# Kernel tuning notes

Hardware: AMD Instinct MI355X
Metric: run time of the kernel (lower is better)

The kernel has to match this reference:

```python
import jax, jax.numpy as jnp
import numpy as np

N_NODES = 100000
N_EDGES = 1600000
IN_DIM, HID_DIM, LAT_DIM = 256, 128, 64


def setup_inputs() -> dict:
    key = jax.random.key(0)
    ks = jax.random.split(key, 10)
    x = jax.random.normal(ks[0], (N_NODES, IN_DIM), dtype=jnp.float32)
    edge_index = jax.random.randint(ks[1], (2, N_EDGES), 0, N_NODES, dtype=jnp.int32)
    s = 1.0 / np.sqrt(IN_DIM)
    W1 = jax.random.normal(ks[2], (IN_DIM, HID_DIM), dtype=jnp.float32) * s
    b1 = jnp.zeros((HID_DIM,), dtype=jnp.float32)
    s2 = 1.0 / np.sqrt(HID_DIM)
    Wmu = jax.random.normal(ks[3], (HID_DIM, LAT_DIM), dtype=jnp.float32) * s2
    bmu = jnp.zeros((LAT_DIM,), dtype=jnp.float32)
    Wls = jax.random.normal(ks[4], (HID_DIM, LAT_DIM), dtype=jnp.float32) * s2
    bls = jnp.zeros((LAT_DIM,), dtype=jnp.float32)
    eps = jax.random.normal(ks[5], (N_NODES, LAT_DIM), dtype=jnp.float32)
    return {"x": x, "edge_index": edge_index, "W1": W1, "b1": b1,
            "Wmu": Wmu, "bmu": bmu, "Wls": Wls, "bls": bls, "eps": eps}


def _gcn_norm(edge_index, n_nodes):
    # PyG GCNConv: add self-loops, symmetric normalization D^-1/2 A D^-1/2
    loops = jnp.arange(n_nodes, dtype=edge_index.dtype)
    src = jnp.concatenate([edge_index[0], loops])
    dst = jnp.concatenate([edge_index[1], loops])
    ones = jnp.ones(src.shape[0], dtype=jnp.float32)
    deg = jax.ops.segment_sum(ones, dst, num_segments=n_nodes)
    dinv = jnp.where(deg > 0, jax.lax.rsqrt(deg), 0.0)
    norm = dinv[src] * dinv[dst]  # [E + N]
    return src, dst, norm


def _gcn_conv(x, src, dst, norm, W, b, n_nodes):
    h = x @ W                       # transform first (in_dim >= out_dim)
    msg = h[src] * norm[:, None]    # gather + scale per edge
    out = jax.ops.segment_sum(msg, dst, num_segments=n_nodes)  # scatter-add
    return out + b


def reference(x, edge_index, W1, b1, Wmu, bmu, Wls, bls, eps):
    n = x.shape[0]
    src, dst, norm = _gcn_norm(edge_index, n)
    hidden = jax.nn.relu(_gcn_conv(x, src, dst, norm, W1, b1, n))
    mu = _gcn_conv(hidden, src, dst, norm, Wmu, bmu, n)
    logstd = _gcn_conv(hidden, src, dst, norm, Wls, bls, n)
    # reparameterize (training mode): z = mu + eps * exp(logstd)
    z = mu + eps * jnp.exp(logstd)
    return (z, mu, logstd)
```

## Files before the change

kernel.cpp:

```cpp
#include <hip/hip_runtime.h>
#include <cstdint>
#include <cstddef>

typedef __attribute__((ext_vector_type(8))) short short8v;
typedef __attribute__((ext_vector_type(4))) float f32x4;

#define BSHIFT 9
#define NBUCK_MAX 256
#define BCAP 16384
#define F8SCALE 16.0f
#define F8INV   0.0625f

__device__ __forceinline__ unsigned short f2bf_rne(float x) {
    unsigned int u = __float_as_uint(x);
    return (unsigned short)((u + 0x7fffu + ((u >> 16) & 1u)) >> 16);
}

__device__ __forceinline__ short8v pack_bf16x8(float4 a, float4 b) {
    unsigned int u0, u1, u2, u3;
    asm("v_cvt_pk_bf16_f32 %0, %1, %2" : "=v"(u0) : "v"(a.x), "v"(a.y));
    asm("v_cvt_pk_bf16_f32 %0, %1, %2" : "=v"(u1) : "v"(a.z), "v"(a.w));
    asm("v_cvt_pk_bf16_f32 %0, %1, %2" : "=v"(u2) : "v"(b.x), "v"(b.y));
    asm("v_cvt_pk_bf16_f32 %0, %1, %2" : "=v"(u3) : "v"(b.z), "v"(b.w));
    uint4 r = make_uint4(u0, u1, u2, u3);
    return *(short8v*)&r;
}

__device__ __forceinline__ unsigned int pk_fp8(float a, float b, float c, float d) {
    int r = 0;
    r = __builtin_amdgcn_cvt_pk_fp8_f32(a, b, r, false);
    r = __builtin_amdgcn_cvt_pk_fp8_f32(c, d, r, true);
    return (unsigned int)r;
}
__device__ __forceinline__ void accf8(float* a, uint2 v) {
    auto p0 = __builtin_amdgcn_cvt_pk_f32_fp8((int)v.x, false);
    auto p1 = __builtin_amdgcn_cvt_pk_f32_fp8((int)v.x, true);
    auto p2 = __builtin_amdgcn_cvt_pk_f32_fp8((int)v.y, false);
    auto p3 = __builtin_amdgcn_cvt_pk_f32_fp8((int)v.y, true);
    a[0] += p0[0]; a[1] += p0[1];
    a[2] += p1[0]; a[3] += p1[1];
    a[4] += p2[0]; a[5] += p2[1];
    a[6] += p3[0]; a[7] += p3[1];
}


__global__ __launch_bounds__(256) void k_prepB(const float* __restrict__ W1,
                                               const float* __restrict__ Wmu,
                                               const float* __restrict__ Wls,
                                               unsigned short* __restrict__ B1h,
                                               unsigned short* __restrict__ B2t,
                                               int* __restrict__ bcur) {
    int i = blockIdx.x * 256 + threadIdx.x;
    if (blockIdx.x == 0 && threadIdx.x < NBUCK_MAX) bcur[threadIdx.x] = 0;
    if (i < 256 * 128) {
        int k = i >> 7, c = i & 127;
        int ch = ((c & 15) << 3) | (c >> 4);
        B1h[c * 256 + k] = f2bf_rne(W1[k * 128 + ch]);
    }
    if (i < 128 * 128) {
        int k = i >> 7, och = i & 127;
        float vv = (och < 64) ? Wmu[k * 64 + och] : Wls[k * 64 + (och - 64)];
        B2t[och * 128 + k] = f2bf_rne(vv);
    }
}


__global__ __launch_bounds__(256) void k_scatb(const int* __restrict__ srcv,
                                               const int* __restrict__ dstv,
                                               int* __restrict__ bcur,
                                               unsigned int* __restrict__ ebuf, int E) {
    __shared__ int hcnt[NBUCK_MAX], hbase[NBUCK_MAX], hcur[NBUCK_MAX];
    int t = threadIdx.x;
    for (int b = t; b < NBUCK_MAX; b += 256) { hcnt[b] = 0; hcur[b] = 0; }
    __syncthreads();
    int base = blockIdx.x * 4096;
    for (int q = 0; q < 16; ++q) {
        int i = base + q * 256 + t;
        if (i < E) atomicAdd(&hcnt[dstv[i] >> BSHIFT], 1);
    }
    __syncthreads();
    for (int b = t; b < NBUCK_MAX; b += 256)
        hbase[b] = hcnt[b] ? atomicAdd(&bcur[b], hcnt[b]) : 0;
    __syncthreads();
    for (int q = 0; q < 16; ++q) {
        int i = base + q * 256 + t;
        if (i < E) {
            int d = dstv[i], b = d >> BSHIFT;
            int off = hbase[b] + atomicAdd(&hcur[b], 1);
            if (off < BCAP)
                ebuf[(size_t)b * BCAP + off] = ((unsigned)srcv[i] << 9) | (unsigned)(d & 511);
        }
    }
}

__global__ __launch_bounds__(512) void k_bsort(const unsigned int* __restrict__ ebuf,
                                               const int* __restrict__ bcur,
                                               int* __restrict__ colv,
                                               int* __restrict__ rowstart,
                                               int* __restrict__ rowend,
                                               float* __restrict__ dinv, int n) {
    __shared__ int cnt[512], sc[512], cur[512];
    int t = threadIdx.x;
    int b = blockIdx.x;
    int node0 = b << BSHIFT;
    int nn = min(512, n - node0);
    int s0 = (int)((size_t)b * BCAP);
    int total = min(bcur[b], BCAP);
    cnt[t] = 0;
    __syncthreads();
    for (int i = t; i < total; i += 512)
        atomicAdd(&cnt[ebuf[s0 + i] & 511u], 1);
    __syncthreads();
    int v = cnt[t];
    sc[t] = v;
    __syncthreads();
    for (int off = 1; off < 512; off <<= 1) {
        int x = 0;
        if (t >= off) x = sc[t - off];
        __syncthreads();
        if (t >= off) sc[t] += x;
        __syncthreads();
    }
    if (t < nn) {
        int rs = s0 + sc[t] - v;
        cur[t] = rs;
        rowstart[node0 + t] = rs;
        rowend[node0 + t] = rs + v;
        dinv[node0 + t] = rsqrtf((float)(v + 1));
    }
    __syncthreads();
    for (int i = t; i < total; i += 512) {
        unsigned int pv = ebuf[s0 + i];
        int pos = atomicAdd(&cur[pv & 511u], 1);
        colv[pos] = (int)(pv >> 9);
    }
}


__global__ __launch_bounds__(256) void k_gemm1(const float* __restrict__ A,
                                               const unsigned short* __restrict__ Bth,
                                               const float* __restrict__ dinv,
                                               unsigned char* __restrict__ Cf8, int M) {
    const int K = 256;
    __shared__ unsigned short Bs[128 * 128];
    const int tid = threadIdx.x;
    const int w = tid >> 6, l = tid & 63;
    const int lr = l & 15, lq = l >> 4;
    const int row0 = blockIdx.x * 64 + w * 16;

    int rg = row0 + lr;
    const float* ap = A + (size_t)(rg < M ? rg : 0) * K + lq * 8;

    float4 ar[8][2];
#pragma unroll
    for (int s = 0; s < 8; ++s) {
        ar[s][0] = *(const float4*)(ap + s * 32);
        ar[s][1] = *(const float4*)(ap + s * 32 + 4);
    }

    f32x4 acc[8];
#pragma unroll
    for (int ct = 0; ct < 8; ++ct) acc[ct] = (f32x4){0.f, 0.f, 0.f, 0.f};

#pragma unroll
    for (int h = 0; h < 2; ++h) {
        if (h) __syncthreads();
#pragma unroll
        for (int r = 0; r < 8; ++r) {
            int rw = r * 4 + w;
            int sl = rw >> 3, ct = rw & 7;
            short8v v = *(const short8v*)(Bth + (size_t)(ct * 16 + lr) * K + (h * 4 + sl) * 32 + lq * 8);
            *(short8v*)(&Bs[(rw * 64 + l) * 8]) = v;
        }
        __syncthreads();

#pragma unroll
        for (int sl = 0; sl < 4; ++sl) {
            int sg = h * 4 + sl;
            short8v ah = pack_bf16x8(ar[sg][0], ar[sg][1]);
#pragma unroll
            for (int ct = 0; ct < 8; ++ct) {
                short8v bh = *(const short8v*)(&Bs[((sl * 8 + ct) * 64 + l) * 8]);
                acc[ct] = __builtin_amdgcn_mfma_f32_16x16x32_bf16(ah, bh, acc[ct], 0, 0, 0);
            }
        }
    }

    int rbase = row0 + (lq << 2);
#pragma unroll
    for (int j = 0; j < 4; ++j) {
        int row = rbase + j;
        if (row < M) {
            float dv = dinv[row] * F8SCALE;
            uint2 r;
            r.x = pk_fp8(dv * acc[0][j], dv * acc[1][j], dv * acc[2][j], dv * acc[3][j]);
            r.y = pk_fp8(dv * acc[4][j], dv * acc[5][j], dv * acc[6][j], dv * acc[7][j]);
            *(uint2*)(Cf8 + (size_t)row * 128 + lr * 8) = r;
        }
    }
}


__global__ __launch_bounds__(256) void k_prop1(const unsigned char* __restrict__ hf,
                                               const int* __restrict__ colv,
                                               const int* __restrict__ rowstart,
                                               const int* __restrict__ rowend,
                                               const float* __restrict__ dinv,
                                               const float* __restrict__ bias,
                                               unsigned char* __restrict__ of, int n) {
    int wid = (blockIdx.x * 256 + threadIdx.x) >> 6;
    int nid = wid * 4 + ((threadIdx.x >> 4) & 3);
    if (nid >= n) return;
    int cl = threadIdx.x & 15;
    const unsigned char* hp = hf + cl * 8;
    int s = rowstart[nid], e = rowend[nid];
    float a[8] = {0.f, 0.f, 0.f, 0.f, 0.f, 0.f, 0.f, 0.f};
    int i = s;
    for (; i + 4 <= e; i += 4) {
        int c0 = colv[i], c1 = colv[i + 1], c2 = colv[i + 2], c3 = colv[i + 3];
        uint2 v0 = *(const uint2*)(hp + (size_t)c0 * 128);
        uint2 v1 = *(const uint2*)(hp + (size_t)c1 * 128);
        uint2 v2 = *(const uint2*)(hp + (size_t)c2 * 128);
        uint2 v3 = *(const uint2*)(hp + (size_t)c3 * 128);
        accf8(a, v0); accf8(a, v1); accf8(a, v2); accf8(a, v3);
    }
    for (; i < e; ++i) {
        int c = colv[i];
        uint2 v = *(const uint2*)(hp + (size_t)c * 128);
        accf8(a, v);
    }
    uint2 vo = *(const uint2*)(hp + (size_t)nid * 128);
    accf8(a, vo);
    float dv = dinv[nid];
    float din = dv * F8INV;
    float dos = dv * F8SCALE;
    float4 b0 = *(const float4*)(bias + cl * 8);
    float4 b1v = *(const float4*)(bias + cl * 8 + 4);
    float bb[8] = {b0.x, b0.y, b0.z, b0.w, b1v.x, b1v.y, b1v.z, b1v.w};
    float o[8];
#pragma unroll
    for (int k = 0; k < 8; ++k)
        o[k] = fmaxf(a[k] * din + bb[k], 0.f) * dos;
    uint2 r;
    r.x = pk_fp8(o[0], o[1], o[2], o[3]);
    r.y = pk_fp8(o[4], o[5], o[6], o[7]);
    *(uint2*)(of + (size_t)nid * 128 + cl * 8) = r;
}


__global__ __launch_bounds__(256) void k_prop2z(const unsigned char* __restrict__ hf,
                                                const int* __restrict__ colv,
                                                const int* __restrict__ rowstart,
                                                const int* __restrict__ rowend,
                                                const float* __restrict__ dinv,
                                                const unsigned short* __restrict__ B2t,
                                                const float* __restrict__ bmu,
                                                const float* __restrict__ bls,
                                                const float* __restrict__ eps,
                                                float* __restrict__ zout,
                                                float* __restrict__ muout,
                                                float* __restrict__ lsout, int n) {
    __shared__ unsigned short aggb[16][136];
    const int tid = threadIdx.x;
    const int w = tid >> 6, l = tid & 63;
    const int base = blockIdx.x * 16;

    {
        int g = l >> 4, cl = l & 15;
        int slot = w * 4 + g;
        int nid = base + slot;
        float a[8] = {0.f, 0.f, 0.f, 0.f, 0.f, 0.f, 0.f, 0.f};
        float dv = 0.f;
        if (nid < n) {
            const unsigned char* hp = hf + cl * 8;
            int s = rowstart[nid], e = rowend[nid];
            int i = s;
            for (; i + 4 <= e; i += 4) {
                int c0 = colv[i], c1 = colv[i + 1], c2 = colv[i + 2], c3 = colv[i + 3];
                uint2 v0 = *(const uint2*)(hp + (size_t)c0 * 128);
                uint2 v1 = *(const uint2*)(hp + (size_t)c1 * 128);
                uint2 v2 = *(const uint2*)(hp + (size_t)c2 * 128);
                uint2 v3 = *(const uint2*)(hp + (size_t)c3 * 128);
                accf8(a, v0); accf8(a, v1); accf8(a, v2); accf8(a, v3);
            }
            for (; i < e; ++i) {
                int c = colv[i];
                uint2 v = *(const uint2*)(hp + (size_t)c * 128);
                accf8(a, v);
            }
            uint2 vo = *(const uint2*)(hp + (size_t)nid * 128);
            accf8(a, vo);
            dv = dinv[nid] * F8INV;
        }
        short8v r;
#pragma unroll
        for (int k = 0; k < 8; ++k) r[k] = (short)f2bf_rne(a[k] * dv);
        *(short8v*)(&aggb[slot][cl * 8]) = r;
    }
    __syncthreads();

    const int lr = l & 15, lq = l >> 4;
    f32x4 acc0 = (f32x4){0.f, 0.f, 0.f, 0.f};
    f32x4 acc1 = (f32x4){0.f, 0.f, 0.f, 0.f};
#pragma unroll
    for (int sl = 0; sl < 4; ++sl) {
        short8v af = *(const short8v*)(&aggb[lr][sl * 32 + lq * 8]);
        short8v b0 = *(const short8v*)(B2t + (size_t)(w * 16 + lr) * 128 + sl * 32 + lq * 8);
        short8v b1 = *(const short8v*)(B2t + (size_t)((w + 4) * 16 + lr) * 128 + sl * 32 + lq * 8);
        acc0 = __builtin_amdgcn_mfma_f32_16x16x32_bf16(af, b0, acc0, 0, 0, 0);
        acc1 = __builtin_amdgcn_mfma_f32_16x16x32_bf16(af, b1, acc1, 0, 0, 0);
    }

    int och = w * 16 + lr;
    float bmv = bmu[och], blv = bls[och];
#pragma unroll
    for (int j = 0; j < 4; ++j) {
        int nid = base + lq * 4 + j;
        if (nid < n) {
            float mu = acc0[j] + bmv;
            float ls = acc1[j] + blv;
            size_t o = (size_t)nid * 64 + och;
            float z = mu + eps[o] * __expf(ls);
            zout[o] = z;
            muout[o] = mu;
            lsout[o] = ls;
        }
    }
}


extern "C" void kernel_launch(void* const* d_in, const int* in_sizes, int n_in,
                              void* d_out, int out_size, void* d_ws, size_t ws_size,
                              hipStream_t stream) {
    const float* x   = (const float*)d_in[0];
    const int*   ei  = (const int*)d_in[1];
    const float* W1  = (const float*)d_in[2];
    const float* b1  = (const float*)d_in[3];
    const float* Wmu = (const float*)d_in[4];
    const float* bmu = (const float*)d_in[5];
    const float* Wls = (const float*)d_in[6];
    const float* bls = (const float*)d_in[7];
    const float* eps = (const float*)d_in[8];

    const int n = in_sizes[0] / 256;
    const int E = in_sizes[1] / 2;
    const int* srcv = ei;
    const int* dstv = ei + E;
    const int nbuck = (n + 511) >> BSHIFT;

    char* w = (char*)d_ws;
    auto alloc = [&](size_t bytes) -> char* {
        char* p = w;
        w += (bytes + 255) & ~(size_t)255;
        return p;
    };
    float* dinv     = (float*)alloc((size_t)n * 4);
    int*   rowstart = (int*)alloc((size_t)n * 4);
    int*   rowend   = (int*)alloc((size_t)n * 4);
    int*   bcur     = (int*)alloc((size_t)NBUCK_MAX * 4);
    unsigned int* ebuf = (unsigned int*)alloc((size_t)nbuck * BCAP * 4);
    int*   colv     = (int*)alloc((size_t)nbuck * BCAP * 4);
    unsigned short* B1h = (unsigned short*)alloc(128 * 256 * 2);
    unsigned short* B2t = (unsigned short*)alloc(128 * 128 * 2);
    unsigned char* hf8   = (unsigned char*)alloc((size_t)n * 128);
    unsigned char* hidf8 = (unsigned char*)alloc((size_t)n * 128);

    const int ecb = (E + 4095) / 4096;

    k_prepB<<<128, 256, 0, stream>>>(W1, Wmu, Wls, B1h, B2t, bcur);
    k_scatb<<<ecb, 256, 0, stream>>>(srcv, dstv, bcur, ebuf, E);
    k_bsort<<<nbuck, 512, 0, stream>>>(ebuf, bcur, colv, rowstart, rowend, dinv, n);

    k_gemm1<<<(n + 63) / 64, 256, 0, stream>>>(x, B1h, dinv, hf8, n);
    k_prop1<<<(n + 15) / 16, 256, 0, stream>>>(hf8, colv, rowstart, rowend, dinv, b1, hidf8, n);

    float* zout  = (float*)d_out;
    float* muout = zout + (size_t)n * 64;
    float* lsout = muout + (size_t)n * 64;
    k_prop2z<<<(n + 15) / 16, 256, 0, stream>>>(hidf8, colv, rowstart, rowend, dinv,
                                                B2t, bmu, bls, eps,
                                                zout, muout, lsout, n);
}
```

Measured before the change: 189.7 us.

## Make prop2z per-wave independent, removing block barrier in final propagation

Each wave now aggregates its own 16 nodes over four passes into a private shared-memory tile, then computes all 128 output channels with eight MFMA accumulators. This replaces the block-wide __syncthreads with a local LDS wait, and each block now handles 64 nodes instead of 16. The intent is to remove cross-wave stalls caused by uneven node degrees. The cost is less parallelism within each wave during the gather phase, more accumulator registers, and more B2t loads per wave.

```diff
diff --git a/kernel.cpp b/kernel.cpp
--- a/kernel.cpp
+++ b/kernel.cpp
@@ -260,19 +260,19 @@
                                                 float* __restrict__ zout,
                                                 float* __restrict__ muout,
                                                 float* __restrict__ lsout, int n) {
-    __shared__ unsigned short aggb[16][136];
+    __shared__ unsigned short aggb[4][16][136];
     const int tid = threadIdx.x;
     const int w = tid >> 6, l = tid & 63;
-    const int base = blockIdx.x * 16;
-
-    {
-        int g = l >> 4, cl = l & 15;
-        int slot = w * 4 + g;
-        int nid = base + slot;
+    const int wbase = blockIdx.x * 64 + w * 16;
+
+    const int g = (l >> 4) & 3, cl = l & 15;
+    const unsigned char* hp = hf + cl * 8;
+    for (int p = 0; p < 4; ++p) {
+        int slot = p * 4 + g;
+        int nid = wbase + slot;
         float a[8] = {0.f, 0.f, 0.f, 0.f, 0.f, 0.f, 0.f, 0.f};
         float dv = 0.f;
         if (nid < n) {
-            const unsigned char* hp = hf + cl * 8;
             int s = rowstart[nid], e = rowend[nid];
             int i = s;
             for (; i + 4 <= e; i += 4) {
@@ -295,35 +295,41 @@
         short8v r;
 #pragma unroll
         for (int k = 0; k < 8; ++k) r[k] = (short)f2bf_rne(a[k] * dv);
-        *(short8v*)(&aggb[slot][cl * 8]) = r;
-    }
-    __syncthreads();
+        *(short8v*)(&aggb[w][slot][cl * 8]) = r;
+    }
+    asm volatile("s_waitcnt lgkmcnt(0)" ::: "memory");
+    __builtin_amdgcn_sched_barrier(0);
 
     const int lr = l & 15, lq = l >> 4;
-    f32x4 acc0 = (f32x4){0.f, 0.f, 0.f, 0.f};
-    f32x4 acc1 = (f32x4){0.f, 0.f, 0.f, 0.f};
+    f32x4 accD[8];
+#pragma unroll
+    for (int t = 0; t < 8; ++t) accD[t] = (f32x4){0.f, 0.f, 0.f, 0.f};
 #pragma unroll
     for (int sl = 0; sl < 4; ++sl) {
-        short8v af = *(const short8v*)(&aggb[lr][sl * 32 + lq * 8]);
-        short8v b0 = *(const short8v*)(B2t + (size_t)(w * 16 + lr) * 128 + sl * 32 + lq * 8);
-        short8v b1 = *(const short8v*)(B2t + (size_t)((w + 4) * 16 + lr) * 128 + sl * 32 + lq * 8);
-        acc0 = __builtin_amdgcn_mfma_f32_16x16x32_bf16(af, b0, acc0, 0, 0, 0);
-        acc1 = __builtin_amdgcn_mfma_f32_16x16x32_bf16(af, b1, acc1, 0, 0, 0);
-    }
-
-    int och = w * 16 + lr;
-    float bmv = bmu[och], blv = bls[och];
-#pragma unroll
-    for (int j = 0; j < 4; ++j) {
-        int nid = base + lq * 4 + j;
-        if (nid < n) {
-            float mu = acc0[j] + bmv;
-            float ls = acc1[j] + blv;
-            size_t o = (size_t)nid * 64 + och;
-            float z = mu + eps[o] * __expf(ls);
-            zout[o] = z;
-            muout[o] = mu;
-            lsout[o] = ls;
+        short8v af = *(const short8v*)(&aggb[w][lr][sl * 32 + lq * 8]);
+#pragma unroll
+        for (int t = 0; t < 8; ++t) {
+            short8v bt = *(const short8v*)(B2t + (size_t)(t * 16 + lr) * 128 + sl * 32 + lq * 8);
+            accD[t] = __builtin_amdgcn_mfma_f32_16x16x32_bf16(af, bt, accD[t], 0, 0, 0);
+        }
+    }
+
+#pragma unroll
+    for (int t = 0; t < 4; ++t) {
+        int och = t * 16 + lr;
+        float bmv = bmu[och], blv = bls[och];
+#pragma unroll
+        for (int j = 0; j < 4; ++j) {
+            int nid = wbase + lq * 4 + j;
+            if (nid < n) {
+                float mu = accD[t][j] + bmv;
+                float ls = accD[t + 4][j] + blv;
+                size_t o = (size_t)nid * 64 + och;
+                float z = mu + eps[o] * __expf(ls);
+                zout[o] = z;
+                muout[o] = mu;
+                lsout[o] = ls;
+            }
         }
     }
 }
@@ -377,7 +383,7 @@
     float* zout  = (float*)d_out;
     float* muout = zout + (size_t)n * 64;
     float* lsout = muout + (size_t)n * 64;
-    k_prop2z<<<(n + 15) / 16, 256, 0, stream>>>(hidf8, colv, rowstart, rowend, dinv,
+    k_prop2z<<<(n + 63) / 64, 256, 0, stream>>>(hidf8, colv, rowstart, rowend, dinv,
                                                 B2t, bmu, bls, eps,
                                                 zout, muout, lsout, n);
 }
```

After: 211.9 us. +11.7%, slower.
